# Kernel tuning notes

Hardware: AMD Instinct MI355X
Metric: run time of the kernel (lower is better)

The kernel has to match this reference:

```python
import jax, jax.numpy as jnp
import numpy as np

DIM = 128
NUM_HEADS = 8
HEAD_DIM = DIM // NUM_HEADS
SCALE = HEAD_DIM ** -0.5


def _attn_branch(xs, Wq, bq, Wp, bp):
    # xs: (N, L, C) batch of sequences; Q=K=V=q (per the module)
    N, L, C = xs.shape
    q = xs @ Wq + bq                                   # (N, L, C)
    q = q.reshape(N, L, NUM_HEADS, HEAD_DIM).transpose(0, 2, 1, 3)  # (N, h, L, d)
    qs = q * SCALE
    attn = jax.nn.softmax(jnp.einsum('nhld,nhmd->nhlm', qs, qs), axis=-1)
    out = jnp.einsum('nhlm,nhmd->nhld', attn, q)       # (N, h, L, d)
    out = out.transpose(0, 2, 1, 3).reshape(N, L, C)
    return out @ Wp + bp


def setup_inputs() -> dict:
    key = jax.random.key(0)
    ks = jax.random.split(key, 12)
    B, C, D, H, W = 1, DIM, 31, 32, 32
    s = 0.02
    return {
        'x': jax.random.normal(ks[0], (B, C, D, H, W), jnp.float32),
        'Wq_spec': jax.random.normal(ks[1], (C, C), jnp.float32) * s,
        'bq_spec': jnp.zeros((C,), jnp.float32),
        'Wp_spec': jax.random.normal(ks[2], (C, C), jnp.float32) * s,
        'bp_spec': jnp.zeros((C,), jnp.float32),
        'Wq_spat': jax.random.normal(ks[3], (C, C), jnp.float32) * s,
        'bq_spat': jnp.zeros((C,), jnp.float32),
        'Wp_spat': jax.random.normal(ks[4], (C, C), jnp.float32) * s,
        'bp_spat': jnp.zeros((C,), jnp.float32),
        'Wg': jax.random.normal(ks[5], (2 * C, C), jnp.float32) * s,
        'bg': jnp.zeros((C,), jnp.float32),
    }


def reference(x, Wq_spec, bq_spec, Wp_spec, bp_spec,
              Wq_spat, bq_spat, Wp_spat, bp_spat, Wg, bg):
    B, C, D, H, W = x.shape
    # ---- spectral branch: sequences of length D per spatial position ----
    x_spec = x.transpose(0, 3, 4, 2, 1).reshape(B * H * W, D, C)
    out_spec = _attn_branch(x_spec, Wq_spec, bq_spec, Wp_spec, bp_spec)
    out_spectral = out_spec.reshape(B, H, W, D, C).transpose(0, 4, 3, 1, 2)  # (B,C,D,H,W)
    # ---- spatial branch: sequences of length H*W per band ----
    x_spat = x.transpose(0, 2, 3, 4, 1).reshape(B * D, H * W, C)
    out_spat = _attn_branch(x_spat, Wq_spat, bq_spat, Wp_spat, bp_spat)
    out_spatial = out_spat.reshape(B, D, H, W, C).transpose(0, 4, 1, 2, 3)   # (B,C,D,H,W)
    # ---- sigmoid-gated fusion (global average pooled gate) ----
    gi = jnp.concatenate([
        out_spectral.mean(axis=(2, 3, 4)),
        out_spatial.mean(axis=(2, 3, 4)),
    ], axis=-1)                                          # (B, 2C)
    gate = jax.nn.sigmoid(gi @ Wg + bg)[:, :, None, None, None]  # (B,C,1,1,1)
    return gate * out_spectral + (1.0 - gate) * out_spatial
```

## Files before the change

### kernel.cpp

```cpp
#include <hip/hip_runtime.h>
#include <cstddef>

#define CC 128
#define NH 8
#define HD 16
#define DDIM 31
#define HWW 1024
#define TOK 31744
#define SCALE2 0.0625f
#define QTOK 64

typedef __attribute__((ext_vector_type(4))) short  short4v;
typedef __attribute__((ext_vector_type(8))) short  short8v;
typedef __attribute__((ext_vector_type(4))) float  float4v;
typedef __attribute__((ext_vector_type(2))) unsigned uint2v;
typedef __attribute__((ext_vector_type(8))) __bf16 bf16x8;

__device__ inline unsigned bf16rne(float f) {
    unsigned u = __float_as_uint(f);
    return (u + 0x7fffu + ((u >> 16) & 1u)) >> 16;
}
__device__ inline float bf2f(unsigned h) { return __uint_as_float(h << 16); }

__device__ inline unsigned packsplit(float v) {
    unsigned h = bf16rne(v);
    unsigned l = bf16rne(v - bf2f(h));
    return h | (l << 16);
}
__device__ inline uint2 pack_hi4(uint4 p) {
    return make_uint2((p.x & 0xffffu) | (p.y << 16),
                      (p.z & 0xffffu) | (p.w << 16));
}
__device__ inline uint2 pack_lo4(uint4 p) {
    return make_uint2((p.x >> 16) | (p.y & 0xffff0000u),
                      (p.z >> 16) | (p.w & 0xffff0000u));
}

__device__ inline short4v pack_pf(unsigned u0, unsigned u1,
                                  unsigned u2, unsigned u3) {
    uint2v pd;
    pd[0] = __builtin_amdgcn_perm(u1, u0, 0x07060302u);
    pd[1] = __builtin_amdgcn_perm(u3, u2, 0x07060302u);
    return __builtin_bit_cast(short4v, pd);
}

__device__ inline float4v mfma32(short8v a, short8v b, float4v c) {
    return __builtin_amdgcn_mfma_f32_16x16x32_bf16(
        __builtin_bit_cast(bf16x8, a), __builtin_bit_cast(bf16x8, b), c, 0, 0, 0);
}

#define AST 136
#define WPL (CC * CC)

__global__ __launch_bounds__(256) void wprep_kernel(
    const float* __restrict__ Wq1, const float* __restrict__ Wq2,
    const float* __restrict__ Wp1, const float* __restrict__ Wp2,
    ushort* __restrict__ wplanes)
{
    const int m = blockIdx.x >> 4;
    const int e = (blockIdx.x & 15) * 256 + threadIdx.x;
    const int co = e >> 5, kb = e & 31;
    const float* W = (m == 0) ? Wq1 : (m == 1) ? Wq2 : (m == 2) ? Wp1 : Wp2;
    ushort* hi = wplanes + (size_t)m * 2 * WPL;
    ushort* lo = hi + WPL;
    ushort hv[4], lv[4];
#pragma unroll
    for (int j = 0; j < 4; ++j) {
        float w = W[(size_t)(kb * 4 + j) * CC + co];
        unsigned h = bf16rne(w);
        hv[j] = (ushort)h;
        lv[j] = (ushort)bf16rne(w - bf2f(h));
    }
    *(uint2*)&hi[(size_t)co * CC + kb * 4] =
        make_uint2((unsigned)hv[0] | ((unsigned)hv[1] << 16),
                   (unsigned)hv[2] | ((unsigned)hv[3] << 16));
    *(uint2*)&lo[(size_t)co * CC + kb * 4] =
        make_uint2((unsigned)lv[0] | ((unsigned)lv[1] << 16),
                   (unsigned)lv[2] | ((unsigned)lv[3] << 16));
}

__device__ inline void load_wfrags_p(const ushort* __restrict__ Whi,
                                     const ushort* __restrict__ Wlo,
                                     int co0, int l, int quad,
                                     short8v* ah, short8v* al)
{
    const ushort* rh = Whi + (size_t)(co0 + l) * CC + quad * 8;
    const ushort* rl = Wlo + (size_t)(co0 + l) * CC + quad * 8;
#pragma unroll
    for (int k4 = 0; k4 < 4; ++k4) {
        ah[k4] = *(const short8v*)&rh[k4 * 32];
        al[k4] = *(const short8v*)&rl[k4 * 32];
    }
}

__global__ __launch_bounds__(512, 4) void qproj_kernel(
    const float* __restrict__ x,
    const ushort* __restrict__ wplanes,
    const float* __restrict__ bq1, const float* __restrict__ bq2,
    unsigned* __restrict__ q1p, unsigned* __restrict__ q2p,
    float* __restrict__ sums)
{
    __shared__ ushort sbuf[2 * QTOK * AST];
    ushort* Ahi = sbuf;
    ushort* Alo = sbuf + QTOK * AST;
    unsigned* S = (unsigned*)sbuf;
    const int tid = threadIdx.x;
    const int t0  = blockIdx.x * QTOK;
    if (blockIdx.x == 0 && tid < 2 * CC) sums[tid] = 0.f;

    for (int i = tid; i < QTOK * 32; i += 512) {
        int t = i & 63, c4 = i >> 6;
        unsigned hw[2], lw[2];
#pragma unroll
        for (int p = 0; p < 2; ++p) {
            unsigned h0, l0, h1, l1;
            {
                float v = x[(size_t)(c4 * 4 + p * 2 + 0) * TOK + t0 + t];
                h0 = bf16rne(v); l0 = bf16rne(v - bf2f(h0));
            }
            {
                float v = x[(size_t)(c4 * 4 + p * 2 + 1) * TOK + t0 + t];
                h1 = bf16rne(v); l1 = bf16rne(v - bf2f(h1));
            }
            hw[p] = h0 | (h1 << 16);
            lw[p] = l0 | (l1 << 16);
        }
        *(uint2*)&Ahi[t * AST + c4 * 4] = make_uint2(hw[0], hw[1]);
        *(uint2*)&Alo[t * AST + c4 * 4] = make_uint2(lw[0], lw[1]);
    }
    __syncthreads();

    const int lane = tid & 63;
    const int l    = lane & 15;
    const int quad = lane >> 4;
    const int co0  = (tid >> 6) * 16;

    short8v ah[2][4], al[2][4];
    load_wfrags_p(wplanes,           wplanes + WPL,     co0, l, quad, ah[0], al[0]);
    load_wfrags_p(wplanes + 2 * WPL, wplanes + 3 * WPL, co0, l, quad, ah[1], al[1]);
    float4v acc[2][4];
#pragma unroll
    for (int br = 0; br < 2; ++br)
#pragma unroll
        for (int nt = 0; nt < 4; ++nt) acc[br][nt] = (float4v){0.f, 0.f, 0.f, 0.f};
#pragma unroll
    for (int k4 = 0; k4 < 4; ++k4) {
#pragma unroll
        for (int nt = 0; nt < 4; ++nt) {
            short8v bh = *(const short8v*)&Ahi[(nt * 16 + l) * AST + k4 * 32 + quad * 8];
            short8v bl = *(const short8v*)&Alo[(nt * 16 + l) * AST + k4 * 32 + quad * 8];
            acc[0][nt] = mfma32(ah[0][k4], bh, acc[0][nt]);
            acc[0][nt] = mfma32(ah[0][k4], bl, acc[0][nt]);
            acc[0][nt] = mfma32(al[0][k4], bh, acc[0][nt]);
            acc[1][nt] = mfma32(ah[1][k4], bh, acc[1][nt]);
            acc[1][nt] = mfma32(ah[1][k4], bl, acc[1][nt]);
            acc[1][nt] = mfma32(al[1][k4], bh, acc[1][nt]);
        }
    }

    for (int branch = 0; branch < 2; ++branch) {
        const float* bq = branch ? bq2 : bq1;
        unsigned* op    = branch ? q2p : q1p;
        float4 bv = *(const float4*)&bq[co0 + quad * 4];
        float bb[4] = {bv.x, bv.y, bv.z, bv.w};
        __syncthreads();
#pragma unroll
        for (int nt = 0; nt < 4; ++nt) {
#pragma unroll
            for (int reg = 0; reg < 4; ++reg)
                S[(nt * 16 + l) * AST + co0 + quad * 4 + reg] =
                    packsplit(acc[branch][nt][reg] + bb[reg]);
        }
        __syncthreads();
        for (int i = tid; i < QTOK * 32; i += 512) {
            int t = i >> 5, c4 = i & 31;
            uint4 pv = *(const uint4*)&S[t * AST + c4 * 4];
            *(uint4*)&op[(size_t)(t0 + t) * CC + c4 * 4] = pv;
        }
    }
}

#define QS2 132
#define QSS 20
#define QTP 1044
__global__ __launch_bounds__(1024, 4) void attn_kernel(
    unsigned* __restrict__ q1p, unsigned* __restrict__ q2p,
    float* __restrict__ sums)
{
    __shared__ __align__(16) ushort smem[HWW * QSS + HD * QTP];
    __shared__ float fsum[CC];
    const int tid  = threadIdx.x;
    const int lane = tid & 63;
    const int l    = lane & 15;
    const int quad = lane >> 4;
    const float k2 = SCALE2 * 1.44269504f;
    const short4v onesb = {(short)0x3F80, (short)0x3F80, (short)0x3F80, (short)0x3F80};
    if (tid < CC) fsum[tid] = 0.f;

    {
        const int d = blockIdx.x >> 3, h = blockIdx.x & 7;
        ushort* Qs  = smem;
        ushort* QTs = smem + HWW * QSS;
        const size_t base = (size_t)d * HWW * CC + h * HD;

        for (int i = tid; i < HWW * 4; i += 1024) {
            int row = i >> 2, q4 = i & 3;
            uint4 p = *(const uint4*)&q2p[base + (size_t)row * CC + q4 * 4];
            *(uint2*)&Qs[row * QSS + q4 * 4] = pack_hi4(p);
            QTs[(q4 * 4 + 0) * QTP + row] = (ushort)p.x;
            QTs[(q4 * 4 + 1) * QTP + row] = (ushort)p.y;
            QTs[(q4 * 4 + 2) * QTP + row] = (ushort)p.z;
            QTs[(q4 * 4 + 3) * QTP + row] = (ushort)p.w;
        }
        __syncthreads();

        const int Rw = (tid >> 6) * 64;
        short4v qf[4];
#pragma unroll
        for (int lt = 0; lt < 4; ++lt) {
            short4v raw = *(short4v*)&Qs[(Rw + lt * 16 + l) * QSS + quad * 4];
            short4v sc;
#pragma unroll
            for (int e = 0; e < 4; ++e) {
                float f = bf2f((unsigned)(ushort)raw[e]) * k2;
                sc[e] = (short)bf16rne(f);
            }
            qf[lt] = sc;
        }

        float4v acc[4], accs[4];
#pragma unroll
        for (int lt = 0; lt < 4; ++lt) {
            acc[lt]  = (float4v){0.f, 0.f, 0.f, 0.f};
            accs[lt] = (float4v){0.f, 0.f, 0.f, 0.f};
        }

#pragma unroll 2
        for (int mt = 0; mt < 64; ++mt) {
            const int m0 = mt * 16;
            short4v ka = *(short4v*)&Qs[(m0 + l) * QSS + quad * 4];
            short4v vb = *(short4v*)&QTs[l * QTP + m0 + quad * 4];
#pragma unroll
            for (int lt = 0; lt < 4; ++lt) {
                float4v s = __builtin_amdgcn_mfma_f32_16x16x16bf16_1k(
                    ka, qf[lt], (float4v){0.f, 0.f, 0.f, 0.f}, 0, 0, 0);
                unsigned u0 = __float_as_uint(__builtin_amdgcn_exp2f(s[0]));
                unsigned u1 = __float_as_uint(__builtin_amdgcn_exp2f(s[1]));
                unsigned u2 = __float_as_uint(__builtin_amdgcn_exp2f(s[2]));
                unsigned u3 = __float_as_uint(__builtin_amdgcn_exp2f(s[3]));
                short4v pf = pack_pf(u0, u1, u2, u3);
                acc[lt]  = __builtin_amdgcn_mfma_f32_16x16x16bf16_1k(vb, pf, acc[lt], 0, 0, 0);
                accs[lt] = __builtin_amdgcn_mfma_f32_16x16x16bf16_1k(onesb, pf, accs[lt], 0, 0, 0);
            }
        }

        float vsum[4] = {0.f, 0.f, 0.f, 0.f};
#pragma unroll
        for (int lt = 0; lt < 4; ++lt) {
            float inv = 1.f / accs[lt][0];
            int token = Rw + lt * 16 + l;
            float v0 = acc[lt][0] * inv, v1 = acc[lt][1] * inv;
            float v2 = acc[lt][2] * inv, v3 = acc[lt][3] * inv;
            uint4 pv;
            pv.x = packsplit(v0); pv.y = packsplit(v1);
            pv.z = packsplit(v2); pv.w = packsplit(v3);
            *(uint4*)&q2p[base + (size_t)token * CC + quad * 4] = pv;
            vsum[0] += v0; vsum[1] += v1; vsum[2] += v2; vsum[3] += v3;
        }
#pragma unroll
        for (int reg = 0; reg < 4; ++reg) {
            float v = vsum[reg];
            v += __shfl_xor(v, 1); v += __shfl_xor(v, 2);
            v += __shfl_xor(v, 4); v += __shfl_xor(v, 8);
            if (l == 0) atomicAdd(&fsum[quad * 4 + reg], v);
        }
        __syncthreads();
        if (tid < HD) atomicAdd(&sums[CC + h * HD + tid], fsum[tid]);
    }

    const int half_id = blockIdx.x >> 1;
    const bool has_job = (blockIdx.x & 1) ? (half_id < 4) : (half_id < 124);
    if (!has_job) return;
    const int job = (blockIdx.x & 1) ? (124 + half_id) : half_id;
    const int hw0 = job * 8;

    __syncthreads();
    if (tid < CC) fsum[tid] = 0.f;

    const int wave = tid >> 6;
    const int hwl  = wave >> 1;
    const int half = wave & 1;
    const int hw   = hw0 + hwl;
    ushort* Q = smem + hwl * (32 * QS2);
    for (int it = 0; it < 8; ++it) {
        int idx = it * 64 + lane;
        int dd = half * 16 + (idx >> 5), c4 = idx & 31;
        if (dd < 31) {
            uint4 p = *(const uint4*)&q1p[((size_t)dd * HWW + hw) * CC + c4 * 4];
            *(uint2*)&Q[dd * QS2 + c4 * 4] = pack_hi4(p);
        }
    }
    if (half) for (int i = lane; i < 128; i += 64) Q[31 * QS2 + i] = 0;
    __syncthreads();

    const int hh = half * 4;
#pragma unroll
    for (int hl = 0; hl < 4; ++hl) {
        const int hc = (hh + hl) * HD;
        short4v qf[2];
        qf[0] = *(const short4v*)&Q[l * QS2 + hc + quad * 4];
        qf[1] = *(const short4v*)&Q[(16 + l) * QS2 + hc + quad * 4];
        short4v va[2];
#pragma unroll
        for (int j = 0; j < 2; ++j)
#pragma unroll
            for (int jj = 0; jj < 4; ++jj)
                va[j][jj] = (short)Q[(j * 16 + quad * 4 + jj) * QS2 + hc + l];

        float4v o[2]   = {(float4v){0.f,0.f,0.f,0.f}, (float4v){0.f,0.f,0.f,0.f}};
        float4v osr[2] = {(float4v){0.f,0.f,0.f,0.f}, (float4v){0.f,0.f,0.f,0.f}};
#pragma unroll
        for (int j = 0; j < 2; ++j) {
#pragma unroll
            for (int i2 = 0; i2 < 2; ++i2) {
                float4v s = __builtin_amdgcn_mfma_f32_16x16x16bf16_1k(
                    qf[j], qf[i2], (float4v){0.f,0.f,0.f,0.f}, 0, 0, 0);
                unsigned u0 = __float_as_uint(__builtin_amdgcn_exp2f(s[0] * k2));
                unsigned u1 = __float_as_uint(__builtin_amdgcn_exp2f(s[1] * k2));
                unsigned u2 = __float_as_uint(__builtin_amdgcn_exp2f(s[2] * k2));
                unsigned u3 = __float_as_uint(__builtin_amdgcn_exp2f(s[3] * k2));
                if (j == 1 && quad == 3) u3 = 0;
                short4v pf = pack_pf(u0, u1, u2, u3);
                o[i2]   = __builtin_amdgcn_mfma_f32_16x16x16bf16_1k(va[j], pf, o[i2], 0, 0, 0);
                osr[i2] = __builtin_amdgcn_mfma_f32_16x16x16bf16_1k(onesb, pf, osr[i2], 0, 0, 0);
            }
        }
        float vsum[4] = {0.f, 0.f, 0.f, 0.f};
#pragma unroll
        for (int i2 = 0; i2 < 2; ++i2) {
            float inv = 1.f / osr[i2][0];
            int dq = i2 * 16 + l;
            if (dq < 31) {
                uint4 pv;
                float v0 = o[i2][0] * inv, v1 = o[i2][1] * inv;
                float v2 = o[i2][2] * inv, v3 = o[i2][3] * inv;
                pv.x = packsplit(v0); pv.y = packsplit(v1);
                pv.z = packsplit(v2); pv.w = packsplit(v3);
                *(uint4*)&q1p[((size_t)dq * HWW + hw) * CC + hc + quad * 4] = pv;
                vsum[0] += v0; vsum[1] += v1; vsum[2] += v2; vsum[3] += v3;
            }
        }
#pragma unroll
        for (int r = 0; r < 4; ++r) {
            float v = vsum[r];
            v += __shfl_xor(v, 1); v += __shfl_xor(v, 2);
            v += __shfl_xor(v, 4); v += __shfl_xor(v, 8);
            if (l == 0) atomicAdd(&fsum[hc + quad * 4 + r], v);
        }
    }
    __syncthreads();
    if (tid < CC) atomicAdd(&sums[tid], fsum[tid]);
}

__global__ __launch_bounds__(512) void gate_kernel(
    const float* __restrict__ Wp1, const float* __restrict__ Wp2,
    const float* __restrict__ bp1, const float* __restrict__ bp2,
    const float* __restrict__ Wg,  const float* __restrict__ bg,
    const float* __restrict__ sums, float* __restrict__ gfp)
{
    __shared__ float pa[4][CC];
    __shared__ float giv[2 * CC];
    const int tid = threadIdx.x;
    const int part = tid >> 7, c = tid & 127;
    const float* Wp = (part < 2) ? Wp1 : Wp2;
    const float* sp = (part < 2) ? sums : sums + CC;
    const int k0 = (part & 1) * 64;
    float a = 0.f;
    for (int kk = 0; kk < 64; ++kk) {
        int k = k0 + kk;
        a += sp[k] * Wp[(size_t)k * CC + c];
    }
    pa[part][c] = a;
    __syncthreads();
    if (tid < 2 * CC) {
        float m = (tid < CC) ? (pa[0][tid] + pa[1][tid])
                             : (pa[2][tid - CC] + pa[3][tid - CC]);
        float bb = (tid < CC) ? bp1[tid] : bp2[tid - CC];
        giv[tid] = m * (1.f / (float)TOK) + bb;
    }
    __syncthreads();
    float b = 0.f;
    for (int kk = 0; kk < 64; ++kk) {
        int j = part * 64 + kk;
        b += giv[j] * Wg[(size_t)j * CC + c];
    }
    pa[part][c] = b;
    __syncthreads();
    if (tid < CC)
        gfp[tid] = 1.f / (1.f + __expf(-(bg[tid] + pa[0][tid] + pa[1][tid] +
                                        pa[2][tid] + pa[3][tid])));
}

__global__ __launch_bounds__(512, 4) void oproj_kernel(
    const unsigned* __restrict__ q1p, const unsigned* __restrict__ q2p,
    const ushort* __restrict__ wplanes,
    const float* __restrict__ bp1, const float* __restrict__ bp2,
    const float* __restrict__ gfp, float* __restrict__ out)
{
    __shared__ ushort sbuf[2 * 64 * AST];
    ushort* Ahi = sbuf;
    ushort* Alo = sbuf + 64 * AST;
    unsigned* S = (unsigned*)sbuf;
    const int tid = threadIdx.x;
    const int t0  = blockIdx.x * 64;
    const int lane = tid & 63;
    const int l    = lane & 15;
    const int quad = lane >> 4;
    const int co0  = (tid >> 6) * 16;

    float4v acc[2][4];
#pragma unroll
    for (int br = 0; br < 2; ++br)
#pragma unroll
        for (int nt = 0; nt < 4; ++nt) acc[br][nt] = (float4v){0.f, 0.f, 0.f, 0.f};

    for (int br = 0; br < 2; ++br) {
        const unsigned* Ap = br ? q2p : q1p;
        const ushort* Whi = wplanes + (size_t)(2 + br) * 2 * WPL;
        short8v ah[4], al[4];
        load_wfrags_p(Whi, Whi + WPL, co0, l, quad, ah, al);
        if (br) __syncthreads();
        for (int i = tid; i < 64 * 32; i += 512) {
            int t = i >> 5, c4 = i & 31;
            uint4 p = *(const uint4*)&Ap[(size_t)(t0 + t) * CC + c4 * 4];
            *(uint2*)&Ahi[t * AST + c4 * 4] = pack_hi4(p);
            *(uint2*)&Alo[t * AST + c4 * 4] = pack_lo4(p);
        }
        __syncthreads();
#pragma unroll
        for (int k4 = 0; k4 < 4; ++k4) {
#pragma unroll
            for (int nt = 0; nt < 4; ++nt) {
                short8v bh = *(const short8v*)&Ahi[(nt * 16 + l) * AST + k4 * 32 + quad * 8];
                short8v bl = *(const short8v*)&Alo[(nt * 16 + l) * AST + k4 * 32 + quad * 8];
                acc[br][nt] = mfma32(ah[k4], bh, acc[br][nt]);
                acc[br][nt] = mfma32(ah[k4], bl, acc[br][nt]);
                acc[br][nt] = mfma32(al[k4], bh, acc[br][nt]);
            }
        }
    }

    float4 b1 = *(const float4*)&bp1[co0 + quad * 4];
    float4 b2 = *(const float4*)&bp2[co0 + quad * 4];
    float bb1[4] = {b1.x, b1.y, b1.z, b1.w};
    float bb2[4] = {b2.x, b2.y, b2.z, b2.w};
    float4 gv = *(const float4*)&gfp[co0 + quad * 4];
    float gg[4] = {gv.x, gv.y, gv.z, gv.w};

    __syncthreads();
#pragma unroll
    for (int nt = 0; nt < 4; ++nt) {
        int tl = nt * 16 + l;
#pragma unroll
        for (int reg = 0; reg < 4; ++reg) {
            float v = gg[reg] * (acc[0][nt][reg] + bb1[reg]) +
                      (1.f - gg[reg]) * (acc[1][nt][reg] + bb2[reg]);
            S[(co0 + quad * 4 + reg) * 66 + tl] = __float_as_uint(v);
        }
    }
    __syncthreads();
    for (int i = tid; i < 128 * 32; i += 512) {
        int co = i >> 5, t2 = i & 31;
        uint2 v = *(const uint2*)&S[co * 66 + t2 * 2];
        *(uint2*)&out[(size_t)co * TOK + t0 + t2 * 2] = v;
    }
}

extern "C" void kernel_launch(void* const* d_in, const int* in_sizes, int n_in,
                              void* d_out, int out_size, void* d_ws, size_t ws_size,
                              hipStream_t stream)
{
    const float* x   = (const float*)d_in[0];
    const float* Wq1 = (const float*)d_in[1];
    const float* bq1 = (const float*)d_in[2];
    const float* Wp1 = (const float*)d_in[3];
    const float* bp1 = (const float*)d_in[4];
    const float* Wq2 = (const float*)d_in[5];
    const float* bq2 = (const float*)d_in[6];
    const float* Wp2 = (const float*)d_in[7];
    const float* bp2 = (const float*)d_in[8];
    const float* Wg  = (const float*)d_in[9];
    const float* bg  = (const float*)d_in[10];
    float* out = (float*)d_out;

    const size_t plane = (size_t)TOK * CC;
    unsigned* q1p = (unsigned*)d_ws;
    unsigned* q2p = q1p + plane;
    float*   sums = (float*)(q2p + plane);
    float*   gfp  = sums + 2 * CC;
    ushort*  wpl  = (ushort*)(gfp + CC);

    const size_t need = 2 * plane * sizeof(unsigned) +
                        (2 * CC + CC) * sizeof(float) +
                        (size_t)4 * 2 * WPL * sizeof(ushort);
    if (ws_size < need) return;

    wprep_kernel<<<dim3(64), 256, 0, stream>>>(Wq1, Wq2, Wp1, Wp2, wpl);
    qproj_kernel<<<dim3(TOK / QTOK), 512, 0, stream>>>(x, wpl, bq1, bq2,
                                                       q1p, q2p, sums);
    attn_kernel<<<dim3(248), 1024, 0, stream>>>(q1p, q2p, sums);
    gate_kernel<<<dim3(1), 512, 0, stream>>>(Wp1, Wp2, bp1, bp2, Wg, bg,
                                             sums, gfp);
    oproj_kernel<<<dim3(496), 512, 0, stream>>>(q1p, q2p, wpl,
                                                bp1, bp2, gfp, out);
}
```

Measured before the change: 177.0 us.

## Rebalance spectral attention work across blocks and merge projection staging phases

The attention kernel now launches 256 blocks. Every block handles the spectral attention for 4 spatial positions, with each wave covering 2 heads, replacing the old uneven job split in which odd blocks were mostly idle. The q-projection epilogue stages both branches in a doubled shared buffer behind one barrier. The output projection loads both weight sets and both activation tiles up front, removing the per-branch sync. The larger shared buffers can lower occupancy in the two projection kernels.

```diff
diff --git a/kernel.cpp b/kernel.cpp
--- a/kernel.cpp
+++ b/kernel.cpp
@@ -100,7 +100,7 @@
     unsigned* __restrict__ q1p, unsigned* __restrict__ q2p,
     float* __restrict__ sums)
 {
-    __shared__ ushort sbuf[2 * QTOK * AST];
+    __shared__ ushort sbuf[4 * QTOK * AST];
     ushort* Ahi = sbuf;
     ushort* Alo = sbuf + QTOK * AST;
     unsigned* S = (unsigned*)sbuf;
@@ -158,25 +158,26 @@
         }
     }
 
-    for (int branch = 0; branch < 2; ++branch) {
-        const float* bq = branch ? bq2 : bq1;
-        unsigned* op    = branch ? q2p : q1p;
-        float4 bv = *(const float4*)&bq[co0 + quad * 4];
-        float bb[4] = {bv.x, bv.y, bv.z, bv.w};
-        __syncthreads();
-#pragma unroll
-        for (int nt = 0; nt < 4; ++nt) {
+    float4 bv1 = *(const float4*)&bq1[co0 + quad * 4];
+    float4 bv2 = *(const float4*)&bq2[co0 + quad * 4];
+    float bb[2][4] = {{bv1.x, bv1.y, bv1.z, bv1.w},
+                      {bv2.x, bv2.y, bv2.z, bv2.w}};
+    __syncthreads();
+#pragma unroll
+    for (int br = 0; br < 2; ++br)
+#pragma unroll
+        for (int nt = 0; nt < 4; ++nt)
 #pragma unroll
             for (int reg = 0; reg < 4; ++reg)
-                S[(nt * 16 + l) * AST + co0 + quad * 4 + reg] =
-                    packsplit(acc[branch][nt][reg] + bb[reg]);
-        }
-        __syncthreads();
-        for (int i = tid; i < QTOK * 32; i += 512) {
-            int t = i >> 5, c4 = i & 31;
-            uint4 pv = *(const uint4*)&S[t * AST + c4 * 4];
-            *(uint4*)&op[(size_t)(t0 + t) * CC + c4 * 4] = pv;
-        }
+                S[br * (QTOK * AST) + (nt * 16 + l) * AST + co0 + quad * 4 + reg] =
+                    packsplit(acc[br][nt][reg] + bb[br][reg]);
+    __syncthreads();
+    for (int i = tid; i < 2 * QTOK * 32; i += 512) {
+        int br = i >> 11, j = i & 2047;
+        int t = j >> 5, c4 = j & 31;
+        unsigned* op = br ? q2p : q1p;
+        uint4 pv = *(const uint4*)&S[br * (QTOK * AST) + t * AST + c4 * 4];
+        *(uint4*)&op[(size_t)(t0 + t) * CC + c4 * 4] = pv;
     }
 }
 
@@ -197,7 +198,7 @@
     const short4v onesb = {(short)0x3F80, (short)0x3F80, (short)0x3F80, (short)0x3F80};
     if (tid < CC) fsum[tid] = 0.f;
 
-    {
+    if (blockIdx.x < 248) {
         const int d = blockIdx.x >> 3, h = blockIdx.x & 7;
         ushort* Qs  = smem;
         ushort* QTs = smem + HWW * QSS;
@@ -276,90 +277,85 @@
         }
         __syncthreads();
         if (tid < HD) atomicAdd(&sums[CC + h * HD + tid], fsum[tid]);
-    }
-
-    const int half_id = blockIdx.x >> 1;
-    const bool has_job = (blockIdx.x & 1) ? (half_id < 4) : (half_id < 124);
-    if (!has_job) return;
-    const int job = (blockIdx.x & 1) ? (124 + half_id) : half_id;
-    const int hw0 = job * 8;
-
-    __syncthreads();
-    if (tid < CC) fsum[tid] = 0.f;
-
-    const int wave = tid >> 6;
-    const int hwl  = wave >> 1;
-    const int half = wave & 1;
-    const int hw   = hw0 + hwl;
-    ushort* Q = smem + hwl * (32 * QS2);
-    for (int it = 0; it < 8; ++it) {
-        int idx = it * 64 + lane;
-        int dd = half * 16 + (idx >> 5), c4 = idx & 31;
-        if (dd < 31) {
-            uint4 p = *(const uint4*)&q1p[((size_t)dd * HWW + hw) * CC + c4 * 4];
-            *(uint2*)&Q[dd * QS2 + c4 * 4] = pack_hi4(p);
-        }
-    }
-    if (half) for (int i = lane; i < 128; i += 64) Q[31 * QS2 + i] = 0;
-    __syncthreads();
-
-    const int hh = half * 4;
-#pragma unroll
-    for (int hl = 0; hl < 4; ++hl) {
-        const int hc = (hh + hl) * HD;
-        short4v qf[2];
-        qf[0] = *(const short4v*)&Q[l * QS2 + hc + quad * 4];
-        qf[1] = *(const short4v*)&Q[(16 + l) * QS2 + hc + quad * 4];
-        short4v va[2];
-#pragma unroll
-        for (int j = 0; j < 2; ++j)
-#pragma unroll
-            for (int jj = 0; jj < 4; ++jj)
-                va[j][jj] = (short)Q[(j * 16 + quad * 4 + jj) * QS2 + hc + l];
-
-        float4v o[2]   = {(float4v){0.f,0.f,0.f,0.f}, (float4v){0.f,0.f,0.f,0.f}};
-        float4v osr[2] = {(float4v){0.f,0.f,0.f,0.f}, (float4v){0.f,0.f,0.f,0.f}};
-#pragma unroll
-        for (int j = 0; j < 2; ++j) {
+        __syncthreads();
+        if (tid < CC) fsum[tid] = 0.f;
+    }
+
+    {
+        const int hw0  = blockIdx.x * 4;
+        const int wave = tid >> 6;
+        const int hwl  = wave >> 2;
+        const int hq   = wave & 3;
+        const int hw   = hw0 + hwl;
+        ushort* Q = smem + hwl * (32 * QS2);
+        for (int it = 0; it < 4; ++it) {
+            int idx = it * 64 + lane;
+            int dd = hq * 8 + (idx >> 5), c4 = idx & 31;
+            if (dd < 31) {
+                uint4 p = *(const uint4*)&q1p[((size_t)dd * HWW + hw) * CC + c4 * 4];
+                *(uint2*)&Q[dd * QS2 + c4 * 4] = pack_hi4(p);
+            }
+        }
+        if (hq == 3) for (int i = lane; i < 128; i += 64) Q[31 * QS2 + i] = 0;
+        __syncthreads();
+
+#pragma unroll
+        for (int hl = 0; hl < 2; ++hl) {
+            const int hc = (hq * 2 + hl) * HD;
+            short4v qf[2];
+            qf[0] = *(const short4v*)&Q[l * QS2 + hc + quad * 4];
+            qf[1] = *(const short4v*)&Q[(16 + l) * QS2 + hc + quad * 4];
+            short4v va[2];
+#pragma unroll
+            for (int j = 0; j < 2; ++j)
+#pragma unroll
+                for (int jj = 0; jj < 4; ++jj)
+                    va[j][jj] = (short)Q[(j * 16 + quad * 4 + jj) * QS2 + hc + l];
+
+            float4v o[2]   = {(float4v){0.f,0.f,0.f,0.f}, (float4v){0.f,0.f,0.f,0.f}};
+            float4v osr[2] = {(float4v){0.f,0.f,0.f,0.f}, (float4v){0.f,0.f,0.f,0.f}};
+#pragma unroll
+            for (int j = 0; j < 2; ++j) {
+#pragma unroll
+                for (int i2 = 0; i2 < 2; ++i2) {
+                    float4v s = __builtin_amdgcn_mfma_f32_16x16x16bf16_1k(
+                        qf[j], qf[i2], (float4v){0.f,0.f,0.f,0.f}, 0, 0, 0);
+                    unsigned u0 = __float_as_uint(__builtin_amdgcn_exp2f(s[0] * k2));
+                    unsigned u1 = __float_as_uint(__builtin_amdgcn_exp2f(s[1] * k2));
+                    unsigned u2 = __float_as_uint(__builtin_amdgcn_exp2f(s[2] * k2));
+                    unsigned u3 = __float_as_uint(__builtin_amdgcn_exp2f(s[3] * k2));
+                    if (j == 1 && quad == 3) u3 = 0;
+                    short4v pf = pack_pf(u0, u1, u2, u3);
+                    o[i2]   = __builtin_amdgcn_mfma_f32_16x16x16bf16_1k(va[j], pf, o[i2], 0, 0, 0);
+                    osr[i2] = __builtin_amdgcn_mfma_f32_16x16x16bf16_1k(onesb, pf, osr[i2], 0, 0, 0);
+                }
+            }
+            float vsum[4] = {0.f, 0.f, 0.f, 0.f};
 #pragma unroll
             for (int i2 = 0; i2 < 2; ++i2) {
-                float4v s = __builtin_amdgcn_mfma_f32_16x16x16bf16_1k(
-                    qf[j], qf[i2], (float4v){0.f,0.f,0.f,0.f}, 0, 0, 0);
-                unsigned u0 = __float_as_uint(__builtin_amdgcn_exp2f(s[0] * k2));
-                unsigned u1 = __float_as_uint(__builtin_amdgcn_exp2f(s[1] * k2));
-                unsigned u2 = __float_as_uint(__builtin_amdgcn_exp2f(s[2] * k2));
-                unsigned u3 = __float_as_uint(__builtin_amdgcn_exp2f(s[3] * k2));
-                if (j == 1 && quad == 3) u3 = 0;
-                short4v pf = pack_pf(u0, u1, u2, u3);
-                o[i2]   = __builtin_amdgcn_mfma_f32_16x16x16bf16_1k(va[j], pf, o[i2], 0, 0, 0);
-                osr[i2] = __builtin_amdgcn_mfma_f32_16x16x16bf16_1k(onesb, pf, osr[i2], 0, 0, 0);
-            }
-        }
-        float vsum[4] = {0.f, 0.f, 0.f, 0.f};
-#pragma unroll
-        for (int i2 = 0; i2 < 2; ++i2) {
-            float inv = 1.f / osr[i2][0];
-            int dq = i2 * 16 + l;
-            if (dq < 31) {
-                uint4 pv;
-                float v0 = o[i2][0] * inv, v1 = o[i2][1] * inv;
-                float v2 = o[i2][2] * inv, v3 = o[i2][3] * inv;
-                pv.x = packsplit(v0); pv.y = packsplit(v1);
-                pv.z = packsplit(v2); pv.w = packsplit(v3);
-                *(uint4*)&q1p[((size_t)dq * HWW + hw) * CC + hc + quad * 4] = pv;
-                vsum[0] += v0; vsum[1] += v1; vsum[2] += v2; vsum[3] += v3;
-            }
-        }
-#pragma unroll
-        for (int r = 0; r < 4; ++r) {
-            float v = vsum[r];
-            v += __shfl_xor(v, 1); v += __shfl_xor(v, 2);
-            v += __shfl_xor(v, 4); v += __shfl_xor(v, 8);
-            if (l == 0) atomicAdd(&fsum[hc + quad * 4 + r], v);
-        }
-    }
-    __syncthreads();
-    if (tid < CC) atomicAdd(&sums[tid], fsum[tid]);
+                float inv = 1.f / osr[i2][0];
+                int dq = i2 * 16 + l;
+                if (dq < 31) {
+                    uint4 pv;
+                    float v0 = o[i2][0] * inv, v1 = o[i2][1] * inv;
+                    float v2 = o[i2][2] * inv, v3 = o[i2][3] * inv;
+                    pv.x = packsplit(v0); pv.y = packsplit(v1);
+                    pv.z = packsplit(v2); pv.w = packsplit(v3);
+                    *(uint4*)&q1p[((size_t)dq * HWW + hw) * CC + hc + quad * 4] = pv;
+                    vsum[0] += v0; vsum[1] += v1; vsum[2] += v2; vsum[3] += v3;
+                }
+            }
+#pragma unroll
+            for (int r = 0; r < 4; ++r) {
+                float v = vsum[r];
+                v += __shfl_xor(v, 1); v += __shfl_xor(v, 2);
+                v += __shfl_xor(v, 4); v += __shfl_xor(v, 8);
+                if (l == 0) atomicAdd(&fsum[hc + quad * 4 + r], v);
+            }
+        }
+        __syncthreads();
+        if (tid < CC) atomicAdd(&sums[tid], fsum[tid]);
+    }
 }
 
 __global__ __launch_bounds__(512) void gate_kernel(
@@ -407,9 +403,7 @@
     const float* __restrict__ bp1, const float* __restrict__ bp2,
     const float* __restrict__ gfp, float* __restrict__ out)
 {
-    __shared__ ushort sbuf[2 * 64 * AST];
-    ushort* Ahi = sbuf;
-    ushort* Alo = sbuf + 64 * AST;
+    __shared__ ushort sbuf[4 * 64 * AST];
     unsigned* S = (unsigned*)sbuf;
     const int tid = threadIdx.x;
     const int t0  = blockIdx.x * 64;
@@ -418,34 +412,39 @@
     const int quad = lane >> 4;
     const int co0  = (tid >> 6) * 16;
 
+    short8v ah[2][4], al[2][4];
+    load_wfrags_p(wplanes + 4 * WPL, wplanes + 5 * WPL, co0, l, quad, ah[0], al[0]);
+    load_wfrags_p(wplanes + 6 * WPL, wplanes + 7 * WPL, co0, l, quad, ah[1], al[1]);
+
+    for (int i = tid; i < 2 * 64 * 32; i += 512) {
+        int br = i >> 11, j = i & 2047;
+        int t = j >> 5, c4 = j & 31;
+        const unsigned* Ap = br ? q2p : q1p;
+        uint4 p = *(const uint4*)&Ap[(size_t)(t0 + t) * CC + c4 * 4];
+        ushort* AH = sbuf + br * (2 * 64 * AST);
+        *(uint2*)&AH[t * AST + c4 * 4] = pack_hi4(p);
+        *(uint2*)&AH[64 * AST + t * AST + c4 * 4] = pack_lo4(p);
+    }
+    __syncthreads();
+
     float4v acc[2][4];
 #pragma unroll
     for (int br = 0; br < 2; ++br)
 #pragma unroll
         for (int nt = 0; nt < 4; ++nt) acc[br][nt] = (float4v){0.f, 0.f, 0.f, 0.f};
-
+#pragma unroll
     for (int br = 0; br < 2; ++br) {
-        const unsigned* Ap = br ? q2p : q1p;
-        const ushort* Whi = wplanes + (size_t)(2 + br) * 2 * WPL;
-        short8v ah[4], al[4];
-        load_wfrags_p(Whi, Whi + WPL, co0, l, quad, ah, al);
-        if (br) __syncthreads();
-        for (int i = tid; i < 64 * 32; i += 512) {
-            int t = i >> 5, c4 = i & 31;
-            uint4 p = *(const uint4*)&Ap[(size_t)(t0 + t) * CC + c4 * 4];
-            *(uint2*)&Ahi[t * AST + c4 * 4] = pack_hi4(p);
-            *(uint2*)&Alo[t * AST + c4 * 4] = pack_lo4(p);
-        }
-        __syncthreads();
+        const ushort* Ahi = sbuf + br * (2 * 64 * AST);
+        const ushort* Alo = Ahi + 64 * AST;
 #pragma unroll
         for (int k4 = 0; k4 < 4; ++k4) {
 #pragma unroll
             for (int nt = 0; nt < 4; ++nt) {
                 short8v bh = *(const short8v*)&Ahi[(nt * 16 + l) * AST + k4 * 32 + quad * 8];
                 short8v bl = *(const short8v*)&Alo[(nt * 16 + l) * AST + k4 * 32 + quad * 8];
-                acc[br][nt] = mfma32(ah[k4], bh, acc[br][nt]);
-                acc[br][nt] = mfma32(ah[k4], bl, acc[br][nt]);
-                acc[br][nt] = mfma32(al[k4], bh, acc[br][nt]);
+                acc[br][nt] = mfma32(ah[br][k4], bh, acc[br][nt]);
+                acc[br][nt] = mfma32(ah[br][k4], bl, acc[br][nt]);
+                acc[br][nt] = mfma32(al[br][k4], bh, acc[br][nt]);
             }
         }
     }
@@ -508,7 +507,7 @@
     wprep_kernel<<<dim3(64), 256, 0, stream>>>(Wq1, Wq2, Wp1, Wp2, wpl);
     qproj_kernel<<<dim3(TOK / QTOK), 512, 0, stream>>>(x, wpl, bq1, bq2,
                                                        q1p, q2p, sums);
-    attn_kernel<<<dim3(248), 1024, 0, stream>>>(q1p, q2p, sums);
+    attn_kernel<<<dim3(256), 1024, 0, stream>>>(q1p, q2p, sums);
     gate_kernel<<<dim3(1), 512, 0, stream>>>(Wp1, Wp2, bp1, bp2, Wg, bg,
                                              sums, gfp);
     oproj_kernel<<<dim3(496), 512, 0, stream>>>(q1p, q2p, wpl,
```

Result: no change. 179.0 us (+1.1%).
